# Optimization experiments

Measured on AMD Instinct MI355X. Metric: run time of the kernel, lower is better.

Reference implementation:

```python
import jax, jax.numpy as jnp
import numpy as np
from jax.scipy.linalg import solve_triangular

# Production config from MFAWrapper.from_path: 28x28 images, 50 components, 6 factors
B, DFT, K, L = 2048, 784, 50, 6
LOG2PI = float(np.log(2.0 * np.pi))


def setup_inputs() -> dict:
    key = jax.random.key(0)
    k1, k2, k3, k4, k5, k6 = jax.random.split(key, 6)
    X = jax.random.normal(k1, (B, DFT), dtype=jnp.float32)
    J = jax.random.randint(k2, (B, DFT), 0, 2).astype(jnp.int32)  # binary observation mask
    MU = jax.random.normal(k3, (K, DFT), dtype=jnp.float32) * 0.5
    A_fac = jax.random.normal(k4, (K, DFT, L), dtype=jnp.float32) * 0.1  # factor loadings
    log_D = jax.random.normal(k5, (K, DFT), dtype=jnp.float32) * 0.1 - 1.0  # log noise variances
    PI_logits = jax.random.normal(k6, (K,), dtype=jnp.float32)
    return {"X": X, "J": J, "MU": MU, "A_fac": A_fac, "log_D": log_D, "PI_logits": PI_logits}


def _mfa_conditional(X, J, MU, A_fac, log_D, PI_logits):
    """Batched MFA conditional reconstruction given observed features (mask J==1).

    The per-sample torch.nonzero selection is replaced by mask-weighted linear
    algebra: restricting to observed rows of diag(1/D) is identical to zeroing
    the unobserved entries of the weight, so all B samples are conditioned in
    one batched pass instead of a Python loop.
    """
    dtype = X.dtype
    l = A_fac.shape[-1]
    Jf = (J == 1).astype(dtype)                 # [B, Dft]
    inv_D = jnp.exp(-log_D)                     # [K, Dft]
    # masked residual per (sample, component): [B, K, Dft]
    md = (X[:, None, :] - MU[None, :, :]) * Jf[:, None, :]
    # latent posterior precision P = I + A_o^T D_o^{-1} A_o  -> [B, K, L, L]
    P = jnp.einsum('bd,kd,kdi,kdj->bkij', Jf, inv_D, A_fac, A_fac) + jnp.eye(l, dtype=dtype)
    # q = A_o^T D_o^{-1} (x_o - mu_o)  -> [B, K, L]
    q = jnp.einsum('bkd,kd,kdi->bki', md, inv_D, A_fac)
    # per-component log-likelihood of observed features via Woodbury / matrix det lemma
    Lc = jnp.linalg.cholesky(P)                                         # [B, K, L, L]
    y = solve_triangular(Lc, q[..., None], lower=True)[..., 0]          # [B, K, L]
    quad = jnp.einsum('bkd,kd->bk', md * md, inv_D) - jnp.sum(y * y, axis=-1)
    logdet = (2.0 * jnp.sum(jnp.log(jnp.diagonal(Lc, axis1=-2, axis2=-1)), axis=-1)
              + jnp.einsum('bd,kd->bk', Jf, log_D))
    n_obs = jnp.sum(Jf, axis=-1, keepdims=True)                         # [B, 1]
    log_lik = -0.5 * (quad + logdet + n_obs * LOG2PI)                   # [B, K]
    log_resp = jax.nn.log_softmax(PI_logits)[None, :] + log_lik
    c = jnp.argmax(log_resp, axis=-1)                                   # most responsible component, [B]
    # gather per-sample selected component and form the conditional Gaussian in factor form
    P_sel = jnp.take_along_axis(P, c[:, None, None, None], axis=1)[:, 0]  # [B, L, L]
    q_sel = jnp.take_along_axis(q, c[:, None, None], axis=1)[:, 0]        # [B, L]
    A_sel = A_fac[c]                                                      # [B, Dft, L]
    m_z = jnp.linalg.solve(P_sel, q_sel[..., None])[..., 0]               # posterior latent mean [B, L]
    cov_z = jnp.linalg.inv(P_sel)                                         # posterior latent cov [B, L, L]
    Lz = jnp.linalg.cholesky(cov_z)
    M = MU[c] + jnp.einsum('bdi,bi->bd', A_sel, m_z)                      # conditional mean over all features
    A_out = jnp.einsum('bdi,bij->bdj', A_sel, Lz)                         # loadings: cond cov = A_out A_out^T + diag(D_out)
    D_out = jnp.exp(log_D)[c]                                             # [B, Dft]
    Pw = jnp.ones((X.shape[0], 1), dtype)
    return Pw, M, A_out, D_out


def reference(X, J, MU, A_fac, log_D, PI_logits):
    return _mfa_conditional(X, J, MU, A_fac, log_D, PI_logits)
```

## Files before the change

kernel.cpp:

```cpp
#include <hip/hip_runtime.h>
#include <math.h>

#define B_N 2048
#define D_FT 784
#define K_N 50
#define L_N 6
#define LOG2PI_F 1.8378770664093453f

#define OUT_PW 0
#define OUT_M  (B_N)
#define OUT_A  (OUT_M + B_N*D_FT)
#define OUT_D  (OUT_A + B_N*D_FT*6)

#define WS_SCORES 0
#define WS_PQ     (WS_SCORES + K_N*B_N)
#define WS_XT     (WS_PQ + K_N*27*B_N)
#define WS_JBT    (WS_XT + D_FT*B_N)

#define IDX(i,j) ((i)*((i)+1)/2 + (j))

typedef float v2f __attribute__((ext_vector_type(2)));

#define PK_FMA(acc, a, b) asm("v_pk_fma_f32 %0, %1, %2, %0" : "+v"(acc) : "v"(a), "v"(b))

__device__ __forceinline__ void chol6(const float* P, float* L, float* rd, float* sumlog) {
    float sl = 0.f;
    #pragma unroll
    for (int j = 0; j < 6; ++j) {
        float s = P[IDX(j,j)];
        #pragma unroll
        for (int m = 0; m < j; ++m) s -= L[IDX(j,m)] * L[IDX(j,m)];
        float d = sqrtf(s);
        L[IDX(j,j)] = d;
        float r = 1.0f / d;
        rd[j] = r;
        sl += logf(d);
        #pragma unroll
        for (int i = j + 1; i < 6; ++i) {
            float t = P[IDX(i,j)];
            #pragma unroll
            for (int m = 0; m < j; ++m) t -= L[IDX(i,m)] * L[IDX(j,m)];
            L[IDX(i,j)] = t * r;
        }
    }
    *sumlog = sl;
}

__global__ __launch_bounds__(1024) void k_prep(const float* __restrict__ X,
                                               const int* __restrict__ J,
                                               float4* __restrict__ Xt4,
                                               unsigned* __restrict__ JbT) {
    const int bid = blockIdx.x;
    const int tid = threadIdx.x;
    if (bid < 448) {
        __shared__ float4 tile[32][33];
        int tx = tid & 31, ty = tid >> 5;
        int d4b = (bid % 7) * 32;
        int bb  = (bid / 7) * 32;
        int d4 = d4b + tx;
        if (d4 < D_FT / 4)
            tile[ty][tx] = *(const float4*)&X[(size_t)(bb + ty) * D_FT + d4 * 4];
        __syncthreads();
        int d4o = d4b + ty;
        if (d4o < D_FT / 4)
            Xt4[(size_t)d4o * B_N + (bb + tx)] = tile[tx][ty];
    } else {
        int t = (bid - 448) * 1024 + tid;
        int b = t >> 5;
        int w = t & 31;
        if (w >= 25) return;
        int d0 = w * 32;
        int n = D_FT - d0; if (n > 32) n = 32;
        unsigned u = 0;
        for (int j = 0; j < n; ++j)
            u |= (J[(size_t)b * D_FT + d0 + j] != 0 ? 1u : 0u) << j;
        JbT[(size_t)w * B_N + b] = u;
    }
}

__global__ __launch_bounds__(256) void k_jld(const float* __restrict__ logD,
                                             const unsigned* __restrict__ JbT,
                                             float* __restrict__ SJL) {
    __shared__ float ld[800];
    const int k  = blockIdx.x >> 3;
    const int bt = blockIdx.x & 7;
    for (int i = threadIdx.x; i < 800; i += 256)
        ld[i] = (i < D_FT) ? logD[(size_t)k * D_FT + i] : 0.f;
    __syncthreads();
    const int b = bt * 256 + threadIdx.x;
    float jl0 = 0.f, jl1 = 0.f;
    for (int w = 0; w < 25; ++w) {
        unsigned mw = JbT[(size_t)w * B_N + b];
        const float* lw = &ld[w * 32];
        #pragma unroll
        for (int dd = 0; dd < 32; dd += 2) {
            jl0 += ((mw >> dd) & 1u) ? lw[dd] : 0.f;
            jl1 += ((mw >> (dd + 1)) & 1u) ? lw[dd + 1] : 0.f;
        }
    }
    SJL[(size_t)k * B_N + b] = jl0 + jl1;
}

#define ACC_PAIR(pi, dd, x0, x1) do { \
    const float4 f0 = sm4[(size_t)(pi) * 4 + 0]; \
    const float4 f1 = sm4[(size_t)(pi) * 4 + 1]; \
    const float4 f2 = sm4[(size_t)(pi) * 4 + 2]; \
    const float4 f3 = sm4[(size_t)(pi) * 4 + 3]; \
    v2f m2;  m2.x = (float)((mw >> (dd)) & 1u); m2.y = (float)((mw >> ((dd)+1)) & 1u); \
    v2f x2;  x2.x = (x0); x2.y = (x1); \
    v2f sa2;  sa2.x = f3.x;  sa2.y = f3.y; \
    v2f nmu2; nmu2.x = f3.z; nmu2.y = f3.w; \
    v2f xm2 = x2 + nmu2; \
    v2f w2  = m2 * sa2; \
    v2f z2  = w2 * xm2; \
    v2f a0; a0.x = f0.x; a0.y = f0.y;  v2f a1; a1.x = f0.z; a1.y = f0.w; \
    v2f a2; a2.x = f1.x; a2.y = f1.y;  v2f a3; a3.x = f1.z; a3.y = f1.w; \
    v2f a4; a4.x = f2.x; a4.y = f2.y;  v2f a5; a5.x = f2.z; a5.y = f2.w; \
    v2f u0 = m2 * a0, u1 = m2 * a1, u2 = m2 * a2; \
    v2f u3 = m2 * a3, u4 = m2 * a4, u5 = m2 * a5; \
    PK_FMA(Pm2[0],  u0, u0); \
    PK_FMA(Pm2[1],  u1, u0); PK_FMA(Pm2[2],  u1, u1); \
    PK_FMA(Pm2[3],  u2, u0); PK_FMA(Pm2[4],  u2, u1); PK_FMA(Pm2[5],  u2, u2); \
    PK_FMA(Pm2[6],  u3, u0); PK_FMA(Pm2[7],  u3, u1); PK_FMA(Pm2[8],  u3, u2); PK_FMA(Pm2[9],  u3, u3); \
    PK_FMA(Pm2[10], u4, u0); PK_FMA(Pm2[11], u4, u1); PK_FMA(Pm2[12], u4, u2); PK_FMA(Pm2[13], u4, u3); PK_FMA(Pm2[14], u4, u4); \
    PK_FMA(Pm2[15], u5, u0); PK_FMA(Pm2[16], u5, u1); PK_FMA(Pm2[17], u5, u2); PK_FMA(Pm2[18], u5, u3); PK_FMA(Pm2[19], u5, u4); PK_FMA(Pm2[20], u5, u5); \
    PK_FMA(qv2[0], z2, u0); PK_FMA(qv2[1], z2, u1); PK_FMA(qv2[2], z2, u2); \
    PK_FMA(qv2[3], z2, u3); PK_FMA(qv2[4], z2, u4); PK_FMA(qv2[5], z2, u5); \
    PK_FMA(quad2, z2, z2); \
} while (0)

__global__ __launch_bounds__(256, 4) void k_accum(
        const float4* __restrict__ Xt4, const unsigned* __restrict__ JbT,
        const float* __restrict__ A, const float* __restrict__ MU,
        const float* __restrict__ logD, const float* __restrict__ PI,
        float* __restrict__ scores, float* __restrict__ Pq) {
    __shared__ float4 sm4[200 * 4];
    float* smem = (float*)sm4;
    const int k   = blockIdx.x >> 5;
    const int tid = threadIdx.x;
    const int s   = tid & 63;
    const int h   = tid >> 6;
    const int b   = (blockIdx.x & 31) * 64 + s;

    v2f Pm2[21], qv2[6], quad2;
    #pragma unroll
    for (int t = 0; t < 21; ++t) { Pm2[t].x = 0.f; Pm2[t].y = 0.f; }
    #pragma unroll
    for (int t = 0; t < 6; ++t) { qv2[t].x = 0.f; qv2[t].y = 0.f; }
    quad2.x = 0.f; quad2.y = 0.f;
    int nob = 0;

    for (int c = 0; c < 2; ++c) {
        const int dbase = c ? 384 : 0;
        const int npair = c ? 200 : 192;
        __syncthreads();
        for (int p = tid; p < npair; p += 256) {
            const int d0 = dbase + 2 * p;
            const float* ar0 = A + ((size_t)k * D_FT + d0) * 6;
            const float* ar1 = ar0 + 6;
            float sa0 = expf(-0.5f * logD[(size_t)k * D_FT + d0]);
            float sa1 = expf(-0.5f * logD[(size_t)k * D_FT + d0 + 1]);
            float4 f0, f1, f2, f3;
            f0.x = sa0 * ar0[0]; f0.y = sa1 * ar1[0]; f0.z = sa0 * ar0[1]; f0.w = sa1 * ar1[1];
            f1.x = sa0 * ar0[2]; f1.y = sa1 * ar1[2]; f1.z = sa0 * ar0[3]; f1.w = sa1 * ar1[3];
            f2.x = sa0 * ar0[4]; f2.y = sa1 * ar1[4]; f2.z = sa0 * ar0[5]; f2.w = sa1 * ar1[5];
            f3.x = sa0; f3.y = sa1;
            f3.z = -MU[(size_t)k * D_FT + d0];
            f3.w = -MU[(size_t)k * D_FT + d0 + 1];
            sm4[(size_t)p * 4 + 0] = f0;
            sm4[(size_t)p * 4 + 1] = f1;
            sm4[(size_t)p * 4 + 2] = f2;
            sm4[(size_t)p * 4 + 3] = f3;
        }
        __syncthreads();

        const int wb = (c ? 12 : 0) + 3 * h;
        for (int w = wb; w < wb + 3; ++w) {
            const unsigned mw = JbT[(size_t)w * B_N + b];
            nob += __popc(mw);
            const int plb = w * 16 - (dbase >> 1);
            const float4* xp = Xt4 + (size_t)(w * 8) * B_N + b;
            #pragma unroll 2
            for (int g = 0; g < 8; ++g) {
                float4 xv = xp[(size_t)g * B_N];
                ACC_PAIR(plb + 2 * g,     g * 4,     xv.x, xv.y);
                ACC_PAIR(plb + 2 * g + 1, g * 4 + 2, xv.z, xv.w);
            }
        }
        if (c == 1 && h == 3) {
            const unsigned mw = JbT[(size_t)24 * B_N + b];
            nob += __popc(mw);
            const int plb = 24 * 16 - 192;
            const float4* xp = Xt4 + (size_t)(24 * 8) * B_N + b;
            #pragma unroll
            for (int g = 0; g < 4; ++g) {
                float4 xv = xp[(size_t)g * B_N];
                ACC_PAIR(plb + 2 * g,     g * 4,     xv.x, xv.y);
                ACC_PAIR(plb + 2 * g + 1, g * 4 + 2, xv.z, xv.w);
            }
        }
    }

    float Pm[21], qv[6], quad;
    #pragma unroll
    for (int t = 0; t < 21; ++t) Pm[t] = Pm2[t].x + Pm2[t].y;
    #pragma unroll
    for (int t = 0; t < 6; ++t) qv[t] = qv2[t].x + qv2[t].y;
    quad = quad2.x + quad2.y;

    __syncthreads();
    float* red = smem;
    #define SLAB_WR do { float* o = &red[s * 33]; \
        _Pragma("unroll") for (int t = 0; t < 21; ++t) o[t] = Pm[t]; \
        _Pragma("unroll") for (int t = 0; t < 6; ++t) o[21 + t] = qv[t]; \
        o[27] = quad; o[28] = (float)nob; } while (0)
    #define SLAB_ADD do { const float* o = &red[s * 33]; \
        _Pragma("unroll") for (int t = 0; t < 21; ++t) Pm[t] += o[t]; \
        _Pragma("unroll") for (int t = 0; t < 6; ++t) qv[t] += o[21 + t]; \
        quad += o[27]; nob += (int)o[28]; } while (0)

    if (h == 1) SLAB_WR;
    __syncthreads();
    if (h == 0) SLAB_ADD;
    __syncthreads();
    if (h == 3) SLAB_WR;
    __syncthreads();
    if (h == 2) SLAB_ADD;
    __syncthreads();
    if (h == 2) SLAB_WR;
    __syncthreads();
    if (h == 0) {
        SLAB_ADD;
        float nobs = (float)nob;

        float jld = scores[(size_t)k * B_N + b];

        Pm[0] += 1.f; Pm[2] += 1.f; Pm[5] += 1.f; Pm[9] += 1.f; Pm[14] += 1.f; Pm[20] += 1.f;

        float Lm[21], rd[6], sumlog;
        chol6(Pm, Lm, rd, &sumlog);
        float y[6];
        #pragma unroll
        for (int j = 0; j < 6; ++j) {
            float sv = qv[j];
            #pragma unroll
            for (int m = 0; m < j; ++m) sv -= Lm[IDX(j,m)] * y[m];
            y[j] = sv * rd[j];
        }
        float yy = 0.f;
        #pragma unroll
        for (int j = 0; j < 6; ++j) yy += y[j] * y[j];
        float logdet = 2.f * sumlog + jld;
        float ll = -0.5f * ((quad - yy) + logdet + nobs * LOG2PI_F);
        float score = ll + PI[k];

        scores[(size_t)k * B_N + b] = score;
        float* pq = Pq + (size_t)k * 27 * B_N + b;
        #pragma unroll
        for (int t = 0; t < 21; ++t) pq[(size_t)t * B_N] = Pm[t];
        #pragma unroll
        for (int t = 0; t < 6; ++t) pq[(size_t)(21 + t) * B_N] = qv[t];
    }
}

__global__ __launch_bounds__(256) void k_outsel(
        const float* __restrict__ scores, const float* __restrict__ Pq,
        const float* __restrict__ A, const float* __restrict__ MU,
        const float* __restrict__ logD, float* __restrict__ out) {
    __shared__ float smz[6];
    __shared__ float sLz[21];
    __shared__ int sc;
    const int b = blockIdx.x;
    const int tid = threadIdx.x;

    if (tid < 64) {
        float best = scores[b];
        int bc = 0;
        for (int kk = 1; kk < K_N; ++kk) {
            float sv = scores[(size_t)kk * B_N + b];
            if (sv > best) { best = sv; bc = kk; }
        }

        float Pm[21], qv[6];
        const float* pq = Pq + (size_t)bc * 27 * B_N + b;
        #pragma unroll
        for (int t = 0; t < 21; ++t) Pm[t] = pq[(size_t)t * B_N];
        #pragma unroll
        for (int t = 0; t < 6; ++t) qv[t] = pq[(size_t)(21 + t) * B_N];

        float Lm[21], rd[6], dummy;
        chol6(Pm, Lm, rd, &dummy);

        float y[6];
        #pragma unroll
        for (int j = 0; j < 6; ++j) {
            float sv = qv[j];
            #pragma unroll
            for (int m = 0; m < j; ++m) sv -= Lm[IDX(j,m)] * y[m];
            y[j] = sv * rd[j];
        }
        float mz[6];
        #pragma unroll
        for (int ii = 5; ii >= 0; --ii) {
            float sv = y[ii];
            #pragma unroll
            for (int j = ii + 1; j < 6; ++j) sv -= Lm[IDX(j,ii)] * mz[j];
            mz[ii] = sv * rd[ii];
        }
        float Li[21];
        #pragma unroll
        for (int j = 0; j < 6; ++j) {
            Li[IDX(j,j)] = rd[j];
            #pragma unroll
            for (int i = j + 1; i < 6; ++i) {
                float sv = 0.f;
                #pragma unroll
                for (int m = j; m < i; ++m) sv += Lm[IDX(i,m)] * Li[IDX(m,j)];
                Li[IDX(i,j)] = -sv * rd[i];
            }
        }
        float cov[21];
        #pragma unroll
        for (int i = 0; i < 6; ++i) {
            #pragma unroll
            for (int j = 0; j <= i; ++j) {
                float sv = 0.f;
                #pragma unroll
                for (int m = i; m < 6; ++m) sv += Li[IDX(m,i)] * Li[IDX(m,j)];
                cov[IDX(i,j)] = sv;
            }
        }
        float Lz[21], rd2[6];
        chol6(cov, Lz, rd2, &dummy);

        if (tid == 0) {
            sc = bc;
            out[OUT_PW + b] = 1.0f;
            #pragma unroll
            for (int t = 0; t < 6; ++t) smz[t] = mz[t];
            #pragma unroll
            for (int t = 0; t < 21; ++t) sLz[t] = Lz[t];
        }
    }
    __syncthreads();
    const int c = sc;

    for (int d = tid; d < D_FT; d += 256) {
        const float* ar = A + ((size_t)c * D_FT + d) * 6;
        float a[6];
        #pragma unroll
        for (int i = 0; i < 6; ++i) a[i] = ar[i];
        float mu = MU[(size_t)c * D_FT + d];
        float ld = logD[(size_t)c * D_FT + d];
        float m = mu;
        #pragma unroll
        for (int i = 0; i < 6; ++i) m += a[i] * smz[i];
        out[OUT_M + (size_t)b * D_FT + d] = m;
        out[OUT_D + (size_t)b * D_FT + d] = expf(ld);
        float* ao = out + OUT_A + ((size_t)b * D_FT + d) * 6;
        #pragma unroll
        for (int j = 0; j < 6; ++j) {
            float sv = 0.f;
            #pragma unroll
            for (int i = j; i < 6; ++i) sv += a[i] * sLz[IDX(i,j)];
            ao[j] = sv;
        }
    }
}

extern "C" void kernel_launch(void* const* d_in, const int* in_sizes, int n_in,
                              void* d_out, int out_size, void* d_ws, size_t ws_size,
                              hipStream_t stream) {
    (void)in_sizes; (void)n_in; (void)out_size; (void)ws_size;
    const float* X    = (const float*)d_in[0];
    const int*   J    = (const int*)d_in[1];
    const float* MU   = (const float*)d_in[2];
    const float* A    = (const float*)d_in[3];
    const float* logD = (const float*)d_in[4];
    const float* PI   = (const float*)d_in[5];
    float* out = (float*)d_out;
    float* ws  = (float*)d_ws;

    float*    scores = ws + WS_SCORES;
    float*    Pq     = ws + WS_PQ;
    float4*   Xt4    = (float4*)(ws + WS_XT);
    unsigned* JbT    = (unsigned*)(ws + WS_JBT);

    k_prep<<<512, 1024, 0, stream>>>(X, J, Xt4, JbT);

    k_jld<<<K_N * 8, 256, 0, stream>>>(logD, JbT, scores);

    k_accum<<<32 * K_N, 256, 0, stream>>>(Xt4, JbT, A, MU, logD, PI, scores, Pq);

    k_outsel<<<B_N, 256, 0, stream>>>(scores, Pq, A, MU, logD, out);
}
```

Measured before the change: 138.7 us.

## Process two samples per thread in k_accum to reuse shared-memory loadings

Each thread in the accumulation kernel now handles two batch samples (b0 and b0+64), so each shared-memory record of loadings, inverse noise and negated mean is read once and used for both samples. The grid is halved and the occupancy hint drops from 4 to 3 blocks per SM to make room for the doubled accumulator registers. The arithmetic is also restructured: shared memory holds raw A and 1/D instead of pre-scaled A, and the mask-weighted products use explicit packed mul/add instructions. The cost is more register pressure, lower occupancy, fewer blocks, and a longer serialized shared-memory reduction with twice as many barriers.

```diff
diff --git a/kernel.cpp b/kernel.cpp
--- a/kernel.cpp
+++ b/kernel.cpp
@@ -22,6 +22,8 @@
 typedef float v2f __attribute__((ext_vector_type(2)));
 
 #define PK_FMA(acc, a, b) asm("v_pk_fma_f32 %0, %1, %2, %0" : "+v"(acc) : "v"(a), "v"(b))
+#define PK_MUL(dst, a, b) asm("v_pk_mul_f32 %0, %1, %2" : "=v"(dst) : "v"(a), "v"(b))
+#define PK_ADD(dst, a, b) asm("v_pk_add_f32 %0, %1, %2" : "=v"(dst) : "v"(a), "v"(b))
 
 __device__ __forceinline__ void chol6(const float* P, float* L, float* rd, float* sumlog) {
     float sl = 0.f;
@@ -101,54 +103,106 @@
     SJL[(size_t)k * B_N + b] = jl0 + jl1;
 }
 
-#define ACC_PAIR(pi, dd, x0, x1) do { \
-    const float4 f0 = sm4[(size_t)(pi) * 4 + 0]; \
-    const float4 f1 = sm4[(size_t)(pi) * 4 + 1]; \
-    const float4 f2 = sm4[(size_t)(pi) * 4 + 2]; \
-    const float4 f3 = sm4[(size_t)(pi) * 4 + 3]; \
-    v2f m2;  m2.x = (float)((mw >> (dd)) & 1u); m2.y = (float)((mw >> ((dd)+1)) & 1u); \
-    v2f x2;  x2.x = (x0); x2.y = (x1); \
-    v2f sa2;  sa2.x = f3.x;  sa2.y = f3.y; \
-    v2f nmu2; nmu2.x = f3.z; nmu2.y = f3.w; \
-    v2f xm2 = x2 + nmu2; \
-    v2f w2  = m2 * sa2; \
-    v2f z2  = w2 * xm2; \
-    v2f a0; a0.x = f0.x; a0.y = f0.y;  v2f a1; a1.x = f0.z; a1.y = f0.w; \
-    v2f a2; a2.x = f1.x; a2.y = f1.y;  v2f a3; a3.x = f1.z; a3.y = f1.w; \
-    v2f a4; a4.x = f2.x; a4.y = f2.y;  v2f a5; a5.x = f2.z; a5.y = f2.w; \
-    v2f u0 = m2 * a0, u1 = m2 * a1, u2 = m2 * a2; \
-    v2f u3 = m2 * a3, u4 = m2 * a4, u5 = m2 * a5; \
-    PK_FMA(Pm2[0],  u0, u0); \
-    PK_FMA(Pm2[1],  u1, u0); PK_FMA(Pm2[2],  u1, u1); \
-    PK_FMA(Pm2[3],  u2, u0); PK_FMA(Pm2[4],  u2, u1); PK_FMA(Pm2[5],  u2, u2); \
-    PK_FMA(Pm2[6],  u3, u0); PK_FMA(Pm2[7],  u3, u1); PK_FMA(Pm2[8],  u3, u2); PK_FMA(Pm2[9],  u3, u3); \
-    PK_FMA(Pm2[10], u4, u0); PK_FMA(Pm2[11], u4, u1); PK_FMA(Pm2[12], u4, u2); PK_FMA(Pm2[13], u4, u3); PK_FMA(Pm2[14], u4, u4); \
-    PK_FMA(Pm2[15], u5, u0); PK_FMA(Pm2[16], u5, u1); PK_FMA(Pm2[17], u5, u2); PK_FMA(Pm2[18], u5, u3); PK_FMA(Pm2[19], u5, u4); PK_FMA(Pm2[20], u5, u5); \
-    PK_FMA(qv2[0], z2, u0); PK_FMA(qv2[1], z2, u1); PK_FMA(qv2[2], z2, u2); \
-    PK_FMA(qv2[3], z2, u3); PK_FMA(qv2[4], z2, u4); PK_FMA(qv2[5], z2, u5); \
-    PK_FMA(quad2, z2, z2); \
+__device__ __forceinline__ void epilogue(float* Pm, float* qv, float quad, float nobs,
+                                         int k, int b, const float* __restrict__ PI,
+                                         float* __restrict__ scores,
+                                         float* __restrict__ Pq) {
+    float jld = scores[(size_t)k * B_N + b];
+
+    Pm[0] += 1.f; Pm[2] += 1.f; Pm[5] += 1.f; Pm[9] += 1.f; Pm[14] += 1.f; Pm[20] += 1.f;
+
+    float Lm[21], rd[6], sumlog;
+    chol6(Pm, Lm, rd, &sumlog);
+    float y[6];
+    #pragma unroll
+    for (int j = 0; j < 6; ++j) {
+        float sv = qv[j];
+        #pragma unroll
+        for (int m = 0; m < j; ++m) sv -= Lm[IDX(j,m)] * y[m];
+        y[j] = sv * rd[j];
+    }
+    float yy = 0.f;
+    #pragma unroll
+    for (int j = 0; j < 6; ++j) yy += y[j] * y[j];
+    float logdet = 2.f * sumlog + jld;
+    float ll = -0.5f * ((quad - yy) + logdet + nobs * LOG2PI_F);
+    float score = ll + PI[k];
+
+    scores[(size_t)k * B_N + b] = score;
+    float* pq = Pq + (size_t)k * 27 * B_N + b;
+    #pragma unroll
+    for (int t = 0; t < 21; ++t) pq[(size_t)t * B_N] = Pm[t];
+    #pragma unroll
+    for (int t = 0; t < 6; ++t) pq[(size_t)(21 + t) * B_N] = qv[t];
+}
+
+#define ACC_PAIR2(pi, dd, xa0, xa1, xb0, xb1) do { \
+    const v2f a0 = srec[(size_t)(pi) * 8 + 0]; \
+    const v2f a1 = srec[(size_t)(pi) * 8 + 1]; \
+    const v2f a2 = srec[(size_t)(pi) * 8 + 2]; \
+    const v2f a3 = srec[(size_t)(pi) * 8 + 3]; \
+    const v2f a4 = srec[(size_t)(pi) * 8 + 4]; \
+    const v2f a5 = srec[(size_t)(pi) * 8 + 5]; \
+    const v2f iD2  = srec[(size_t)(pi) * 8 + 6]; \
+    const v2f nmu2 = srec[(size_t)(pi) * 8 + 7]; \
+    v2f ma2; ma2.x = (float)((mwa >> (dd)) & 1u); ma2.y = (float)((mwa >> ((dd)+1)) & 1u); \
+    v2f mb2; mb2.x = (float)((mwb >> (dd)) & 1u); mb2.y = (float)((mwb >> ((dd)+1)) & 1u); \
+    v2f xa2; xa2.x = (xa0); xa2.y = (xa1); \
+    v2f xb2; xb2.x = (xb0); xb2.y = (xb1); \
+    v2f za2; PK_ADD(za2, xa2, nmu2); \
+    v2f zb2; PK_ADD(zb2, xb2, nmu2); \
+    v2f wa2; PK_MUL(wa2, ma2, iD2); \
+    v2f wb2; PK_MUL(wb2, mb2, iD2); \
+    v2f ta2; PK_MUL(ta2, wa2, za2); \
+    v2f tb2; PK_MUL(tb2, wb2, zb2); \
+    PK_FMA(quadA, ta2, za2); \
+    PK_FMA(quadB, tb2, zb2); \
+    v2f u0, u1, u2v, u3, u4, u5; \
+    PK_MUL(u0, wa2, a0); PK_MUL(u1, wa2, a1); PK_MUL(u2v, wa2, a2); \
+    PK_MUL(u3, wa2, a3); PK_MUL(u4, wa2, a4); PK_MUL(u5, wa2, a5); \
+    PK_FMA(PA[0],  u0, a0); \
+    PK_FMA(PA[1],  u1, a0); PK_FMA(PA[2],  u1, a1); \
+    PK_FMA(PA[3],  u2v, a0); PK_FMA(PA[4],  u2v, a1); PK_FMA(PA[5],  u2v, a2); \
+    PK_FMA(PA[6],  u3, a0); PK_FMA(PA[7],  u3, a1); PK_FMA(PA[8],  u3, a2); PK_FMA(PA[9],  u3, a3); \
+    PK_FMA(PA[10], u4, a0); PK_FMA(PA[11], u4, a1); PK_FMA(PA[12], u4, a2); PK_FMA(PA[13], u4, a3); PK_FMA(PA[14], u4, a4); \
+    PK_FMA(PA[15], u5, a0); PK_FMA(PA[16], u5, a1); PK_FMA(PA[17], u5, a2); PK_FMA(PA[18], u5, a3); PK_FMA(PA[19], u5, a4); PK_FMA(PA[20], u5, a5); \
+    PK_FMA(qA[0], ta2, a0); PK_FMA(qA[1], ta2, a1); PK_FMA(qA[2], ta2, a2); \
+    PK_FMA(qA[3], ta2, a3); PK_FMA(qA[4], ta2, a4); PK_FMA(qA[5], ta2, a5); \
+    PK_MUL(u0, wb2, a0); PK_MUL(u1, wb2, a1); PK_MUL(u2v, wb2, a2); \
+    PK_MUL(u3, wb2, a3); PK_MUL(u4, wb2, a4); PK_MUL(u5, wb2, a5); \
+    PK_FMA(PB[0],  u0, a0); \
+    PK_FMA(PB[1],  u1, a0); PK_FMA(PB[2],  u1, a1); \
+    PK_FMA(PB[3],  u2v, a0); PK_FMA(PB[4],  u2v, a1); PK_FMA(PB[5],  u2v, a2); \
+    PK_FMA(PB[6],  u3, a0); PK_FMA(PB[7],  u3, a1); PK_FMA(PB[8],  u3, a2); PK_FMA(PB[9],  u3, a3); \
+    PK_FMA(PB[10], u4, a0); PK_FMA(PB[11], u4, a1); PK_FMA(PB[12], u4, a2); PK_FMA(PB[13], u4, a3); PK_FMA(PB[14], u4, a4); \
+    PK_FMA(PB[15], u5, a0); PK_FMA(PB[16], u5, a1); PK_FMA(PB[17], u5, a2); PK_FMA(PB[18], u5, a3); PK_FMA(PB[19], u5, a4); PK_FMA(PB[20], u5, a5); \
+    PK_FMA(qB[0], tb2, a0); PK_FMA(qB[1], tb2, a1); PK_FMA(qB[2], tb2, a2); \
+    PK_FMA(qB[3], tb2, a3); PK_FMA(qB[4], tb2, a4); PK_FMA(qB[5], tb2, a5); \
 } while (0)
 
-__global__ __launch_bounds__(256, 4) void k_accum(
+__global__ __launch_bounds__(256, 3) void k_accum(
         const float4* __restrict__ Xt4, const unsigned* __restrict__ JbT,
         const float* __restrict__ A, const float* __restrict__ MU,
         const float* __restrict__ logD, const float* __restrict__ PI,
         float* __restrict__ scores, float* __restrict__ Pq) {
-    __shared__ float4 sm4[200 * 4];
-    float* smem = (float*)sm4;
-    const int k   = blockIdx.x >> 5;
+    __shared__ v2f srec[200 * 8];
+    float* smem = (float*)srec;
+    float4* smf4 = (float4*)srec;
+    const int k   = blockIdx.x >> 4;
     const int tid = threadIdx.x;
     const int s   = tid & 63;
     const int h   = tid >> 6;
-    const int b   = (blockIdx.x & 31) * 64 + s;
-
-    v2f Pm2[21], qv2[6], quad2;
-    #pragma unroll
-    for (int t = 0; t < 21; ++t) { Pm2[t].x = 0.f; Pm2[t].y = 0.f; }
-    #pragma unroll
-    for (int t = 0; t < 6; ++t) { qv2[t].x = 0.f; qv2[t].y = 0.f; }
-    quad2.x = 0.f; quad2.y = 0.f;
-    int nob = 0;
+    const int b0  = (blockIdx.x & 15) * 128 + s;
+    const int b1  = b0 + 64;
+
+    v2f PA[21], qA[6], quadA;
+    v2f PB[21], qB[6], quadB;
+    #pragma unroll
+    for (int t = 0; t < 21; ++t) { PA[t].x = 0.f; PA[t].y = 0.f; PB[t].x = 0.f; PB[t].y = 0.f; }
+    #pragma unroll
+    for (int t = 0; t < 6; ++t) { qA[t].x = 0.f; qA[t].y = 0.f; qB[t].x = 0.f; qB[t].y = 0.f; }
+    quadA.x = 0.f; quadA.y = 0.f; quadB.x = 0.f; quadB.y = 0.f;
+    int noba = 0, nobb = 0;
 
     for (int c = 0; c < 2; ++c) {
         const int dbase = c ? 384 : 0;
@@ -158,109 +212,102 @@
             const int d0 = dbase + 2 * p;
             const float* ar0 = A + ((size_t)k * D_FT + d0) * 6;
             const float* ar1 = ar0 + 6;
-            float sa0 = expf(-0.5f * logD[(size_t)k * D_FT + d0]);
-            float sa1 = expf(-0.5f * logD[(size_t)k * D_FT + d0 + 1]);
+            float iD0 = expf(-logD[(size_t)k * D_FT + d0]);
+            float iD1 = expf(-logD[(size_t)k * D_FT + d0 + 1]);
             float4 f0, f1, f2, f3;
-            f0.x = sa0 * ar0[0]; f0.y = sa1 * ar1[0]; f0.z = sa0 * ar0[1]; f0.w = sa1 * ar1[1];
-            f1.x = sa0 * ar0[2]; f1.y = sa1 * ar1[2]; f1.z = sa0 * ar0[3]; f1.w = sa1 * ar1[3];
-            f2.x = sa0 * ar0[4]; f2.y = sa1 * ar1[4]; f2.z = sa0 * ar0[5]; f2.w = sa1 * ar1[5];
-            f3.x = sa0; f3.y = sa1;
+            f0.x = ar0[0]; f0.y = ar1[0]; f0.z = ar0[1]; f0.w = ar1[1];
+            f1.x = ar0[2]; f1.y = ar1[2]; f1.z = ar0[3]; f1.w = ar1[3];
+            f2.x = ar0[4]; f2.y = ar1[4]; f2.z = ar0[5]; f2.w = ar1[5];
+            f3.x = iD0; f3.y = iD1;
             f3.z = -MU[(size_t)k * D_FT + d0];
             f3.w = -MU[(size_t)k * D_FT + d0 + 1];
-            sm4[(size_t)p * 4 + 0] = f0;
-            sm4[(size_t)p * 4 + 1] = f1;
-            sm4[(size_t)p * 4 + 2] = f2;
-            sm4[(size_t)p * 4 + 3] = f3;
+            smf4[(size_t)p * 4 + 0] = f0;
+            smf4[(size_t)p * 4 + 1] = f1;
+            smf4[(size_t)p * 4 + 2] = f2;
+            smf4[(size_t)p * 4 + 3] = f3;
         }
         __syncthreads();
 
         const int wb = (c ? 12 : 0) + 3 * h;
         for (int w = wb; w < wb + 3; ++w) {
-            const unsigned mw = JbT[(size_t)w * B_N + b];
-            nob += __popc(mw);
+            const unsigned mwa = JbT[(size_t)w * B_N + b0];
+            const unsigned mwb = JbT[(size_t)w * B_N + b1];
+            noba += __popc(mwa);
+            nobb += __popc(mwb);
             const int plb = w * 16 - (dbase >> 1);
-            const float4* xp = Xt4 + (size_t)(w * 8) * B_N + b;
+            const float4* xp = Xt4 + (size_t)(w * 8) * B_N + b0;
             #pragma unroll 2
             for (int g = 0; g < 8; ++g) {
-                float4 xv = xp[(size_t)g * B_N];
-                ACC_PAIR(plb + 2 * g,     g * 4,     xv.x, xv.y);
-                ACC_PAIR(plb + 2 * g + 1, g * 4 + 2, xv.z, xv.w);
+                float4 xva = xp[(size_t)g * B_N];
+                float4 xvb = xp[(size_t)g * B_N + 64];
+                ACC_PAIR2(plb + 2 * g,     g * 4,     xva.x, xva.y, xvb.x, xvb.y);
+                ACC_PAIR2(plb + 2 * g + 1, g * 4 + 2, xva.z, xva.w, xvb.z, xvb.w);
             }
         }
         if (c == 1 && h == 3) {
-            const unsigned mw = JbT[(size_t)24 * B_N + b];
-            nob += __popc(mw);
+            const unsigned mwa = JbT[(size_t)24 * B_N + b0];
+            const unsigned mwb = JbT[(size_t)24 * B_N + b1];
+            noba += __popc(mwa);
+            nobb += __popc(mwb);
             const int plb = 24 * 16 - 192;
-            const float4* xp = Xt4 + (size_t)(24 * 8) * B_N + b;
+            const float4* xp = Xt4 + (size_t)(24 * 8) * B_N + b0;
             #pragma unroll
             for (int g = 0; g < 4; ++g) {
-                float4 xv = xp[(size_t)g * B_N];
-                ACC_PAIR(plb + 2 * g,     g * 4,     xv.x, xv.y);
-                ACC_PAIR(plb + 2 * g + 1, g * 4 + 2, xv.z, xv.w);
+                float4 xva = xp[(size_t)g * B_N];
+                float4 xvb = xp[(size_t)g * B_N + 64];
+                ACC_PAIR2(plb + 2 * g,     g * 4,     xva.x, xva.y, xvb.x, xvb.y);
+                ACC_PAIR2(plb + 2 * g + 1, g * 4 + 2, xva.z, xva.w, xvb.z, xvb.w);
             }
         }
     }
 
-    float Pm[21], qv[6], quad;
-    #pragma unroll
-    for (int t = 0; t < 21; ++t) Pm[t] = Pm2[t].x + Pm2[t].y;
-    #pragma unroll
-    for (int t = 0; t < 6; ++t) qv[t] = qv2[t].x + qv2[t].y;
-    quad = quad2.x + quad2.y;
+    float Pa[21], qa[6], quada, Pb[21], qb[6], quadb;
+    #pragma unroll
+    for (int t = 0; t < 21; ++t) { Pa[t] = PA[t].x + PA[t].y; Pb[t] = PB[t].x + PB[t].y; }
+    #pragma unroll
+    for (int t = 0; t < 6; ++t) { qa[t] = qA[t].x + qA[t].y; qb[t] = qB[t].x + qB[t].y; }
+    quada = quadA.x + quadA.y;
+    quadb = quadB.x + quadB.y;
 
     __syncthreads();
     float* red = smem;
-    #define SLAB_WR do { float* o = &red[s * 33]; \
-        _Pragma("unroll") for (int t = 0; t < 21; ++t) o[t] = Pm[t]; \
-        _Pragma("unroll") for (int t = 0; t < 6; ++t) o[21 + t] = qv[t]; \
-        o[27] = quad; o[28] = (float)nob; } while (0)
-    #define SLAB_ADD do { const float* o = &red[s * 33]; \
-        _Pragma("unroll") for (int t = 0; t < 21; ++t) Pm[t] += o[t]; \
-        _Pragma("unroll") for (int t = 0; t < 6; ++t) qv[t] += o[21 + t]; \
-        quad += o[27]; nob += (int)o[28]; } while (0)
-
-    if (h == 1) SLAB_WR;
-    __syncthreads();
-    if (h == 0) SLAB_ADD;
-    __syncthreads();
-    if (h == 3) SLAB_WR;
-    __syncthreads();
-    if (h == 2) SLAB_ADD;
-    __syncthreads();
-    if (h == 2) SLAB_WR;
-    __syncthreads();
-    if (h == 0) {
-        SLAB_ADD;
-        float nobs = (float)nob;
-
-        float jld = scores[(size_t)k * B_N + b];
-
-        Pm[0] += 1.f; Pm[2] += 1.f; Pm[5] += 1.f; Pm[9] += 1.f; Pm[14] += 1.f; Pm[20] += 1.f;
-
-        float Lm[21], rd[6], sumlog;
-        chol6(Pm, Lm, rd, &sumlog);
-        float y[6];
-        #pragma unroll
-        for (int j = 0; j < 6; ++j) {
-            float sv = qv[j];
-            #pragma unroll
-            for (int m = 0; m < j; ++m) sv -= Lm[IDX(j,m)] * y[m];
-            y[j] = sv * rd[j];
-        }
-        float yy = 0.f;
-        #pragma unroll
-        for (int j = 0; j < 6; ++j) yy += y[j] * y[j];
-        float logdet = 2.f * sumlog + jld;
-        float ll = -0.5f * ((quad - yy) + logdet + nobs * LOG2PI_F);
-        float score = ll + PI[k];
-
-        scores[(size_t)k * B_N + b] = score;
-        float* pq = Pq + (size_t)k * 27 * B_N + b;
-        #pragma unroll
-        for (int t = 0; t < 21; ++t) pq[(size_t)t * B_N] = Pm[t];
-        #pragma unroll
-        for (int t = 0; t < 6; ++t) pq[(size_t)(21 + t) * B_N] = qv[t];
-    }
+    #define SLAB_WR(P_, Q_, QU_, NB_) do { float* o = &red[s * 33]; \
+        _Pragma("unroll") for (int t = 0; t < 21; ++t) o[t] = P_[t]; \
+        _Pragma("unroll") for (int t = 0; t < 6; ++t) o[21 + t] = Q_[t]; \
+        o[27] = QU_; o[28] = (float)(NB_); } while (0)
+    #define SLAB_ADD(P_, Q_, QU_, NB_) do { const float* o = &red[s * 33]; \
+        _Pragma("unroll") for (int t = 0; t < 21; ++t) P_[t] += o[t]; \
+        _Pragma("unroll") for (int t = 0; t < 6; ++t) Q_[t] += o[21 + t]; \
+        QU_ += o[27]; NB_ += (int)o[28]; } while (0)
+
+    if (h == 1) SLAB_WR(Pa, qa, quada, noba);
+    __syncthreads();
+    if (h == 0) SLAB_ADD(Pa, qa, quada, noba);
+    __syncthreads();
+    if (h == 3) SLAB_WR(Pa, qa, quada, noba);
+    __syncthreads();
+    if (h == 2) SLAB_ADD(Pa, qa, quada, noba);
+    __syncthreads();
+    if (h == 2) SLAB_WR(Pa, qa, quada, noba);
+    __syncthreads();
+    if (h == 0) SLAB_ADD(Pa, qa, quada, noba);
+    __syncthreads();
+    if (h == 0) SLAB_WR(Pb, qb, quadb, nobb);
+    __syncthreads();
+    if (h == 1) SLAB_ADD(Pb, qb, quadb, nobb);
+    __syncthreads();
+    if (h == 2) SLAB_WR(Pb, qb, quadb, nobb);
+    __syncthreads();
+    if (h == 3) SLAB_ADD(Pb, qb, quadb, nobb);
+    __syncthreads();
+    if (h == 3) SLAB_WR(Pb, qb, quadb, nobb);
+    __syncthreads();
+    if (h == 1) SLAB_ADD(Pb, qb, quadb, nobb);
+
+    if (h == 0)
+        epilogue(Pa, qa, quada, (float)noba, k, b0, PI, scores, Pq);
+    else if (h == 1)
+        epilogue(Pb, qb, quadb, (float)nobb, k, b1, PI, scores, Pq);
 }
 
 __global__ __launch_bounds__(256) void k_outsel(
@@ -390,7 +437,7 @@
 
     k_jld<<<K_N * 8, 256, 0, stream>>>(logD, JbT, scores);
 
-    k_accum<<<32 * K_N, 256, 0, stream>>>(Xt4, JbT, A, MU, logD, PI, scores, Pq);
+    k_accum<<<16 * K_N, 256, 0, stream>>>(Xt4, JbT, A, MU, logD, PI, scores, Pq);
 
     k_outsel<<<B_N, 256, 0, stream>>>(scores, Pq, A, MU, logD, out);
 }
```

Result: slower. 150.9 us (+8.8%).
